# Kernel tuning notes

Measured on AMD Instinct MI355X. Metric: run time of the kernel, lower is better.

## Reference

```python
import jax, jax.numpy as jnp
import numpy as np

K = 32          # init k
E = 0.003       # EMA rate e


def setup_inputs() -> dict:
    key = jax.random.key(0)
    k1, _ = jax.random.split(key)
    features = jax.random.normal(k1, (512, 6, 8192), dtype=jnp.float32)
    threshold = jnp.zeros((1,), dtype=jnp.float32)
    return {"features": features, "threshold": threshold}


def reference(features, threshold):
    batch_size, n_layers, d_features = features.shape
    batch_k = K * batch_size * n_layers
    flat = features.reshape(-1)                      # [B*L*D]
    topk_vals, topk_idxs = jax.lax.top_k(flat, batch_k)
    topk_vals = jax.nn.relu(topk_vals)
    out = jnp.zeros_like(flat).at[topk_idxs].set(topk_vals)
    out = out.reshape(batch_size, n_layers, d_features)
    min_k = jax.lax.stop_gradient(jnp.min(topk_vals))
    new_threshold = (1.0 - E) * threshold + E * min_k
    return out, new_threshold
```

## Files before the change

### kernel.cpp

```cpp
#include <hip/hip_runtime.h>
#include <stdint.h>

#define K_TOTAL   98304u
#define EMA_RATE  0.003f

#define SBINS      16384
#define SBIN_SHIFT 18
#define SAMPLE_VEC 131072
#define STARGET    8192u
#define P2_BINS    4096
#define P2_SHIFT   12
#define LCAP       1024
#define CAP2       65536u
#define EQCAP      256

__device__ __forceinline__ unsigned f2key(float x) {
    unsigned u = __float_as_uint(x);
    return (u & 0x80000000u) ? ~u : (u | 0x80000000u);
}
__device__ __forceinline__ float key2f(unsigned key) {
    unsigned u = (key & 0x80000000u) ? (key & 0x7FFFFFFFu) : ~key;
    return __uint_as_float(u);
}

__global__ __launch_bounds__(256) void sample_hist_kernel(
        const float4* __restrict__ in, unsigned* __restrict__ shist) {
    __shared__ unsigned h[SBINS];
    for (int i = threadIdx.x; i < SBINS; i += 256) h[i] = 0;
    __syncthreads();
    int stride = gridDim.x * 256;
    for (int i = blockIdx.x * 256 + threadIdx.x; i < SAMPLE_VEC; i += stride) {
        float4 v = in[i];
        atomicAdd(&h[f2key(v.x) >> SBIN_SHIFT], 1u);
        atomicAdd(&h[f2key(v.y) >> SBIN_SHIFT], 1u);
        atomicAdd(&h[f2key(v.z) >> SBIN_SHIFT], 1u);
        atomicAdd(&h[f2key(v.w) >> SBIN_SHIFT], 1u);
    }
    __syncthreads();
    for (int i = threadIdx.x; i < SBINS; i += 256) {
        unsigned c = h[i];
        if (c) atomicAdd(&shist[i], c);
    }
}

__global__ __launch_bounds__(256) void sample_scan_kernel(
        const unsigned* __restrict__ shist, unsigned* __restrict__ res) {
    __shared__ unsigned psum[256];
    const int GB = SBINS / 256;
    int t = threadIdx.x;
    int hi = SBINS - 1 - t * GB;
    unsigned s = 0;
    for (int j = 0; j < GB; ++j) s += shist[hi - j];
    psum[t] = s;
    __syncthreads();
    for (int off = 1; off < 256; off <<= 1) {
        unsigned o = (t >= off) ? psum[t - off] : 0u;
        __syncthreads();
        psum[t] += o;
        __syncthreads();
    }
    unsigned cum = psum[t] - s;
    for (int j = 0; j < GB; ++j) {
        unsigned c = shist[hi - j];
        if (cum < STARGET && cum + c >= STARGET) {
            unsigned bin = (unsigned)(hi - j);
            unsigned bb = (bin > 0) ? bin - 1 : 0;
            res[0] = bb << SBIN_SHIFT;
        }
        cum += c;
    }
}

__global__ __launch_bounds__(256) void main_pass_kernel(
        const float4* __restrict__ in, const unsigned* __restrict__ res,
        float* __restrict__ cval, unsigned* __restrict__ cidx,
        unsigned* __restrict__ gcnt, unsigned* __restrict__ ghist,
        unsigned cap, int nvec) {
    __shared__ unsigned h[P2_BINS];
    __shared__ float    lval[LCAP];
    __shared__ unsigned lidx[LCAP];
    __shared__ unsigned lcnt, lbase;
    for (int i = threadIdx.x; i < P2_BINS; i += 256) h[i] = 0;
    if (threadIdx.x == 0) lcnt = 0;
    __syncthreads();
    unsigned base = res[0];
    int stride = gridDim.x * 256;
    for (int i = blockIdx.x * 256 + threadIdx.x; i < nvec; i += stride) {
        float4 v = in[i];
        unsigned idx = 4u * (unsigned)i;
        #pragma unroll
        for (int c = 0; c < 4; ++c) {
            float x = (c == 0) ? v.x : (c == 1) ? v.y : (c == 2) ? v.z : v.w;
            unsigned key = f2key(x);
            if (key >= base) {
                unsigned g = (key - base) >> P2_SHIFT;
                if (g > P2_BINS - 1) g = P2_BINS - 1;
                atomicAdd(&h[g], 1u);
                unsigned p = atomicAdd(&lcnt, 1u);
                if (p < LCAP) { lval[p] = x; lidx[p] = idx + c; }
                else {
                    unsigned q = atomicAdd(gcnt, 1u);
                    if (q < cap) { cval[q] = x; cidx[q] = idx + c; }
                }
            }
        }
    }
    __syncthreads();
    unsigned n = min(lcnt, (unsigned)LCAP);
    if (threadIdx.x == 0) lbase = atomicAdd(gcnt, n);
    __syncthreads();
    for (unsigned j = threadIdx.x; j < n; j += 256) {
        unsigned p = lbase + j;
        if (p < cap) { cval[p] = lval[j]; cidx[p] = lidx[j]; }
    }
    for (int i = threadIdx.x; i < P2_BINS; i += 256) {
        unsigned c = h[i];
        if (c) atomicAdd(&ghist[i], c);
    }
}

__global__ __launch_bounds__(256) void find_g_kernel(
        const unsigned* __restrict__ ghist, unsigned* __restrict__ res2) {
    __shared__ unsigned psum[256];
    const int GB = P2_BINS / 256;
    int t = threadIdx.x;
    int hi = P2_BINS - 1 - t * GB;
    unsigned s = 0;
    for (int j = 0; j < GB; ++j) s += ghist[hi - j];
    psum[t] = s;
    __syncthreads();
    for (int off = 1; off < 256; off <<= 1) {
        unsigned o = (t >= off) ? psum[t - off] : 0u;
        __syncthreads();
        psum[t] += o;
        __syncthreads();
    }
    unsigned cum = psum[t] - s;
    for (int j = 0; j < GB; ++j) {
        unsigned c = ghist[hi - j];
        if (cum < K_TOTAL && cum + c >= K_TOTAL) {
            res2[0] = (unsigned)(hi - j);
            res2[1] = K_TOTAL - cum;
        }
        cum += c;
    }
}

__global__ __launch_bounds__(256) void scatter_kernel(
        const float* __restrict__ cval, const unsigned* __restrict__ cidx,
        const unsigned* __restrict__ gcnt, const unsigned* __restrict__ res,
        const unsigned* __restrict__ res2,
        float* __restrict__ cval2, unsigned* __restrict__ cidx2,
        unsigned* __restrict__ cnt2, unsigned cap,
        float* __restrict__ out) {
    unsigned nc = min(*gcnt, cap);
    unsigned base = res[0];
    unsigned gstar = res2[0];
    int stride = gridDim.x * 256;
    for (unsigned i = blockIdx.x * 256 + threadIdx.x; i < nc; i += stride) {
        float x = cval[i];
        unsigned key = f2key(x);
        unsigned g = (key - base) >> P2_SHIFT;
        if (g > P2_BINS - 1) g = P2_BINS - 1;
        if (g > gstar) {
            out[cidx[i]] = fmaxf(x, 0.0f);
        } else if (g == gstar) {
            unsigned p = atomicAdd(cnt2, 1u);
            if (p < CAP2) { cval2[p] = x; cidx2[p] = cidx[i]; }
        }
    }
}

__global__ __launch_bounds__(256) void final_kernel(
        const float* __restrict__ cval2, const unsigned* __restrict__ cidx2,
        const unsigned* __restrict__ cnt2,
        const unsigned* __restrict__ res, const unsigned* __restrict__ res2,
        float* __restrict__ out,
        const float* __restrict__ thr_in, float* __restrict__ thr_out) {
    __shared__ unsigned h[1 << P2_SHIFT];
    __shared__ unsigned psum[256];
    __shared__ unsigned eqidx[EQCAP];
    __shared__ unsigned eqcnt;
    __shared__ unsigned sh_low, sh_need3;
    const int NB = 1 << P2_SHIFT;
    int t = threadIdx.x;
    unsigned nc2   = min(*cnt2, CAP2);
    unsigned base3 = res[0] + (res2[0] << P2_SHIFT);
    unsigned need2 = res2[1];

    for (int i = t; i < NB; i += 256) h[i] = 0;
    if (t == 0) eqcnt = 0;
    __syncthreads();
    for (unsigned i = t; i < nc2; i += 256) {
        unsigned low = f2key(cval2[i]) - base3;
        if (low > (unsigned)(NB - 1)) low = NB - 1;
        atomicAdd(&h[low], 1u);
    }
    __syncthreads();

    const int GB = NB / 256;
    int hi = NB - 1 - t * GB;
    unsigned s = 0;
    for (int j = 0; j < GB; ++j) s += h[hi - j];
    psum[t] = s;
    __syncthreads();
    for (int off = 1; off < 256; off <<= 1) {
        unsigned o = (t >= off) ? psum[t - off] : 0u;
        __syncthreads();
        psum[t] += o;
        __syncthreads();
    }
    unsigned cum = psum[t] - s;
    for (int j = 0; j < GB; ++j) {
        unsigned c = h[hi - j];
        if (cum < need2 && cum + c >= need2) {
            sh_low = (unsigned)(hi - j);
            sh_need3 = need2 - cum;
        }
        cum += c;
    }
    __syncthreads();
    unsigned kth_key = base3 + sh_low;
    unsigned need3   = sh_need3;

    for (unsigned i = t; i < nc2; i += 256) {
        float x = cval2[i];
        unsigned key = f2key(x);
        if (key > kth_key) {
            out[cidx2[i]] = fmaxf(x, 0.0f);
        } else if (key == kth_key) {
            unsigned p = atomicAdd(&eqcnt, 1u);
            if (p < EQCAP) eqidx[p] = cidx2[i];
        }
    }
    __syncthreads();

    unsigned ne = min(eqcnt, (unsigned)EQCAP);
    float vv = key2f(kth_key);
    for (unsigned e = t; e < ne; e += 256) {
        unsigned my = eqidx[e];
        unsigned rank = 0;
        for (unsigned f = 0; f < ne; ++f) rank += (eqidx[f] < my) ? 1u : 0u;
        if (rank < need3) out[my] = fmaxf(vv, 0.0f);
    }

    if (t == 0) {
        float mink = fmaxf(vv, 0.0f);
        thr_out[0] = (1.0f - EMA_RATE) * thr_in[0] + EMA_RATE * mink;
    }
}

extern "C" void kernel_launch(void* const* d_in, const int* in_sizes, int n_in,
                              void* d_out, int out_size, void* d_ws, size_t ws_size,
                              hipStream_t stream) {
    const float* feat   = (const float*)d_in[0];
    const float* thr_in = (const float*)d_in[1];
    float* out = (float*)d_out;
    int N    = in_sizes[0];
    int nvec = N / 4;

    uint8_t* w = (uint8_t*)d_ws;
    unsigned* shist = (unsigned*)w;
    unsigned* ghist = (unsigned*)(w + (64 << 10));
    unsigned* ctr   = (unsigned*)(w + (80 << 10));
    unsigned* gcnt  = ctr + 0;
    unsigned* cnt2  = ctr + 1;
    unsigned* res   = ctr + 4;
    unsigned* res2  = ctr + 8;

    size_t cand_off = (size_t)1 << 20;
    size_t avail    = (ws_size > cand_off + (CAP2 * 8 + 4096))
                        ? (ws_size - cand_off - CAP2 * 8 - 4096) / 8 : 0;
    unsigned cap = (unsigned)((avail < (size_t)(4u << 20)) ? avail : (size_t)(4u << 20));
    float*    cval  = (float*)(w + cand_off);
    unsigned* cidx  = (unsigned*)(w + cand_off + (size_t)cap * 4);
    float*    cval2 = (float*)(w + cand_off + (size_t)cap * 8);
    unsigned* cidx2 = (unsigned*)(w + cand_off + (size_t)cap * 8 + CAP2 * 4);

    hipMemsetAsync(d_ws, 0, (80 << 10) + 64, stream);
    hipMemsetAsync(d_out, 0, (size_t)N * 4, stream);

    sample_hist_kernel<<<128, 256, 0, stream>>>((const float4*)feat, shist);
    sample_scan_kernel<<<1,   256, 0, stream>>>(shist, res);
    main_pass_kernel  <<<1536, 256, 0, stream>>>((const float4*)feat, res,
                                                 cval, cidx, gcnt, ghist, cap, nvec);
    find_g_kernel     <<<1,   256, 0, stream>>>(ghist, res2);
    scatter_kernel    <<<64,  256, 0, stream>>>(cval, cidx, gcnt, res, res2,
                                                cval2, cidx2, cnt2, cap, out);
    final_kernel      <<<1,   256, 0, stream>>>(cval2, cidx2, cnt2, res, res2,
                                                out, thr_in, out + N);
}
```

Before: 266.3 us.

## Split candidate histogram out of main pass and unroll loads for memory parallelism

Moves the fine histogram off the full-input main pass into a separate kernel that runs only over the compacted candidates. This shrinks main-pass shared memory (no 4096-bin histogram) so more blocks can be resident. The main, sample and scatter loops are unrolled so several float4 loads are in flight per thread, and the single-block scan kernels widen to 1024 threads. The cost is one extra kernel launch and a second read of the candidate array.

```diff
diff --git a/kernel.cpp b/kernel.cpp
--- a/kernel.cpp
+++ b/kernel.cpp
@@ -14,6 +14,9 @@
 #define CAP2       65536u
 #define EQCAP      256
 
+#define MP_BLOCKS  3072
+#define MP_UNROLL  8
+
 __device__ __forceinline__ unsigned f2key(float x) {
     unsigned u = __float_as_uint(x);
     return (u & 0x80000000u) ? ~u : (u | 0x80000000u);
@@ -28,13 +31,23 @@
     __shared__ unsigned h[SBINS];
     for (int i = threadIdx.x; i < SBINS; i += 256) h[i] = 0;
     __syncthreads();
-    int stride = gridDim.x * 256;
-    for (int i = blockIdx.x * 256 + threadIdx.x; i < SAMPLE_VEC; i += stride) {
-        float4 v = in[i];
-        atomicAdd(&h[f2key(v.x) >> SBIN_SHIFT], 1u);
-        atomicAdd(&h[f2key(v.y) >> SBIN_SHIFT], 1u);
-        atomicAdd(&h[f2key(v.z) >> SBIN_SHIFT], 1u);
-        atomicAdd(&h[f2key(v.w) >> SBIN_SHIFT], 1u);
+    unsigned tid = blockIdx.x * 256 + threadIdx.x;
+    unsigned nth = gridDim.x * 256;
+    float4 v[4];
+    #pragma unroll
+    for (int u = 0; u < 4; ++u) {
+        unsigned j = tid + u * nth;
+        v[u] = (j < SAMPLE_VEC) ? in[j] : make_float4(0.f, 0.f, 0.f, 0.f);
+    }
+    #pragma unroll
+    for (int u = 0; u < 4; ++u) {
+        unsigned j = tid + u * nth;
+        if (j < SAMPLE_VEC) {
+            atomicAdd(&h[f2key(v[u].x) >> SBIN_SHIFT], 1u);
+            atomicAdd(&h[f2key(v[u].y) >> SBIN_SHIFT], 1u);
+            atomicAdd(&h[f2key(v[u].z) >> SBIN_SHIFT], 1u);
+            atomicAdd(&h[f2key(v[u].w) >> SBIN_SHIFT], 1u);
+        }
     }
     __syncthreads();
     for (int i = threadIdx.x; i < SBINS; i += 256) {
@@ -43,17 +56,22 @@
     }
 }
 
-__global__ __launch_bounds__(256) void sample_scan_kernel(
+__global__ __launch_bounds__(1024) void sample_scan_kernel(
         const unsigned* __restrict__ shist, unsigned* __restrict__ res) {
-    __shared__ unsigned psum[256];
-    const int GB = SBINS / 256;
+    __shared__ unsigned psum[1024];
+    const int T = 1024;
+    const int GB = SBINS / T;
     int t = threadIdx.x;
     int hi = SBINS - 1 - t * GB;
+    unsigned c[GB];
+    #pragma unroll
+    for (int j = 0; j < GB; ++j) c[j] = shist[hi - j];
     unsigned s = 0;
-    for (int j = 0; j < GB; ++j) s += shist[hi - j];
+    #pragma unroll
+    for (int j = 0; j < GB; ++j) s += c[j];
     psum[t] = s;
     __syncthreads();
-    for (int off = 1; off < 256; off <<= 1) {
+    for (int off = 1; off < T; off <<= 1) {
         unsigned o = (t >= off) ? psum[t - off] : 0u;
         __syncthreads();
         psum[t] += o;
@@ -61,46 +79,50 @@
     }
     unsigned cum = psum[t] - s;
     for (int j = 0; j < GB; ++j) {
-        unsigned c = shist[hi - j];
-        if (cum < STARGET && cum + c >= STARGET) {
+        if (cum < STARGET && cum + c[j] >= STARGET) {
             unsigned bin = (unsigned)(hi - j);
             unsigned bb = (bin > 0) ? bin - 1 : 0;
             res[0] = bb << SBIN_SHIFT;
         }
-        cum += c;
+        cum += c[j];
     }
 }
 
 __global__ __launch_bounds__(256) void main_pass_kernel(
         const float4* __restrict__ in, const unsigned* __restrict__ res,
         float* __restrict__ cval, unsigned* __restrict__ cidx,
-        unsigned* __restrict__ gcnt, unsigned* __restrict__ ghist,
-        unsigned cap, int nvec) {
-    __shared__ unsigned h[P2_BINS];
+        unsigned* __restrict__ gcnt, unsigned cap, int nvec) {
     __shared__ float    lval[LCAP];
     __shared__ unsigned lidx[LCAP];
     __shared__ unsigned lcnt, lbase;
-    for (int i = threadIdx.x; i < P2_BINS; i += 256) h[i] = 0;
     if (threadIdx.x == 0) lcnt = 0;
     __syncthreads();
     unsigned base = res[0];
-    int stride = gridDim.x * 256;
-    for (int i = blockIdx.x * 256 + threadIdx.x; i < nvec; i += stride) {
-        float4 v = in[i];
-        unsigned idx = 4u * (unsigned)i;
-        #pragma unroll
-        for (int c = 0; c < 4; ++c) {
-            float x = (c == 0) ? v.x : (c == 1) ? v.y : (c == 2) ? v.z : v.w;
-            unsigned key = f2key(x);
-            if (key >= base) {
-                unsigned g = (key - base) >> P2_SHIFT;
-                if (g > P2_BINS - 1) g = P2_BINS - 1;
-                atomicAdd(&h[g], 1u);
-                unsigned p = atomicAdd(&lcnt, 1u);
-                if (p < LCAP) { lval[p] = x; lidx[p] = idx + c; }
-                else {
-                    unsigned q = atomicAdd(gcnt, 1u);
-                    if (q < cap) { cval[q] = x; cidx[q] = idx + c; }
+    unsigned tid = blockIdx.x * 256 + threadIdx.x;
+    unsigned nth = gridDim.x * 256;
+    for (unsigned i0 = tid; i0 < (unsigned)nvec; i0 += MP_UNROLL * nth) {
+        float4 v[MP_UNROLL];
+        #pragma unroll
+        for (int u = 0; u < MP_UNROLL; ++u) {
+            unsigned j = i0 + u * nth;
+            v[u] = (j < (unsigned)nvec) ? in[j]
+                   : make_float4(-1e30f, -1e30f, -1e30f, -1e30f);
+        }
+        #pragma unroll
+        for (int u = 0; u < MP_UNROLL; ++u) {
+            unsigned j = i0 + u * nth;
+            unsigned idx = 4u * j;
+            float xs[4] = {v[u].x, v[u].y, v[u].z, v[u].w};
+            #pragma unroll
+            for (int c = 0; c < 4; ++c) {
+                unsigned key = f2key(xs[c]);
+                if (key >= base) {
+                    unsigned p = atomicAdd(&lcnt, 1u);
+                    if (p < LCAP) { lval[p] = xs[c]; lidx[p] = idx + c; }
+                    else {
+                        unsigned q = atomicAdd(gcnt, 1u);
+                        if (q < cap) { cval[q] = xs[c]; cidx[q] = idx + c; }
+                    }
                 }
             }
         }
@@ -113,23 +135,59 @@
         unsigned p = lbase + j;
         if (p < cap) { cval[p] = lval[j]; cidx[p] = lidx[j]; }
     }
+}
+
+__global__ __launch_bounds__(256) void cand_hist_kernel(
+        const float* __restrict__ cval, const unsigned* __restrict__ gcnt,
+        const unsigned* __restrict__ res, unsigned* __restrict__ ghist,
+        unsigned cap) {
+    __shared__ unsigned h[P2_BINS];
+    for (int i = threadIdx.x; i < P2_BINS; i += 256) h[i] = 0;
+    __syncthreads();
+    unsigned nc = min(*gcnt, cap);
+    unsigned base = res[0];
+    unsigned tid = blockIdx.x * 256 + threadIdx.x;
+    unsigned nth = gridDim.x * 256;
+    for (unsigned i0 = tid; i0 < nc; i0 += 4 * nth) {
+        float v[4];
+        #pragma unroll
+        for (int u = 0; u < 4; ++u) {
+            unsigned j = i0 + u * nth;
+            v[u] = (j < nc) ? cval[j] : -1e30f;
+        }
+        #pragma unroll
+        for (int u = 0; u < 4; ++u) {
+            unsigned j = i0 + u * nth;
+            if (j < nc) {
+                unsigned g = (f2key(v[u]) - base) >> P2_SHIFT;
+                if (g > P2_BINS - 1) g = P2_BINS - 1;
+                atomicAdd(&h[g], 1u);
+            }
+        }
+    }
+    __syncthreads();
     for (int i = threadIdx.x; i < P2_BINS; i += 256) {
         unsigned c = h[i];
         if (c) atomicAdd(&ghist[i], c);
     }
 }
 
-__global__ __launch_bounds__(256) void find_g_kernel(
+__global__ __launch_bounds__(1024) void find_g_kernel(
         const unsigned* __restrict__ ghist, unsigned* __restrict__ res2) {
-    __shared__ unsigned psum[256];
-    const int GB = P2_BINS / 256;
+    __shared__ unsigned psum[1024];
+    const int T = 1024;
+    const int GB = P2_BINS / T;
     int t = threadIdx.x;
     int hi = P2_BINS - 1 - t * GB;
+    unsigned c[GB];
+    #pragma unroll
+    for (int j = 0; j < GB; ++j) c[j] = ghist[hi - j];
     unsigned s = 0;
-    for (int j = 0; j < GB; ++j) s += ghist[hi - j];
+    #pragma unroll
+    for (int j = 0; j < GB; ++j) s += c[j];
     psum[t] = s;
     __syncthreads();
-    for (int off = 1; off < 256; off <<= 1) {
+    for (int off = 1; off < T; off <<= 1) {
         unsigned o = (t >= off) ? psum[t - off] : 0u;
         __syncthreads();
         psum[t] += o;
@@ -137,12 +195,11 @@
     }
     unsigned cum = psum[t] - s;
     for (int j = 0; j < GB; ++j) {
-        unsigned c = ghist[hi - j];
-        if (cum < K_TOTAL && cum + c >= K_TOTAL) {
+        if (cum < K_TOTAL && cum + c[j] >= K_TOTAL) {
             res2[0] = (unsigned)(hi - j);
             res2[1] = K_TOTAL - cum;
         }
-        cum += c;
+        cum += c[j];
     }
 }
 
@@ -156,17 +213,28 @@
     unsigned nc = min(*gcnt, cap);
     unsigned base = res[0];
     unsigned gstar = res2[0];
-    int stride = gridDim.x * 256;
-    for (unsigned i = blockIdx.x * 256 + threadIdx.x; i < nc; i += stride) {
-        float x = cval[i];
-        unsigned key = f2key(x);
-        unsigned g = (key - base) >> P2_SHIFT;
-        if (g > P2_BINS - 1) g = P2_BINS - 1;
-        if (g > gstar) {
-            out[cidx[i]] = fmaxf(x, 0.0f);
-        } else if (g == gstar) {
-            unsigned p = atomicAdd(cnt2, 1u);
-            if (p < CAP2) { cval2[p] = x; cidx2[p] = cidx[i]; }
+    unsigned tid = blockIdx.x * 256 + threadIdx.x;
+    unsigned nth = gridDim.x * 256;
+    for (unsigned i0 = tid; i0 < nc; i0 += 4 * nth) {
+        float v[4];
+        #pragma unroll
+        for (int u = 0; u < 4; ++u) {
+            unsigned j = i0 + u * nth;
+            v[u] = (j < nc) ? cval[j] : -1e30f;
+        }
+        #pragma unroll
+        for (int u = 0; u < 4; ++u) {
+            unsigned j = i0 + u * nth;
+            if (j < nc) {
+                unsigned g = (f2key(v[u]) - base) >> P2_SHIFT;
+                if (g > P2_BINS - 1) g = P2_BINS - 1;
+                if (g > gstar) {
+                    out[cidx[j]] = fmaxf(v[u], 0.0f);
+                } else if (g == gstar) {
+                    unsigned p = atomicAdd(cnt2, 1u);
+                    if (p < CAP2) { cval2[p] = v[u]; cidx2[p] = cidx[j]; }
+                }
+            }
         }
     }
 }
@@ -281,11 +349,12 @@
     hipMemsetAsync(d_out, 0, (size_t)N * 4, stream);
 
     sample_hist_kernel<<<128, 256, 0, stream>>>((const float4*)feat, shist);
-    sample_scan_kernel<<<1,   256, 0, stream>>>(shist, res);
-    main_pass_kernel  <<<1536, 256, 0, stream>>>((const float4*)feat, res,
-                                                 cval, cidx, gcnt, ghist, cap, nvec);
-    find_g_kernel     <<<1,   256, 0, stream>>>(ghist, res2);
-    scatter_kernel    <<<64,  256, 0, stream>>>(cval, cidx, gcnt, res, res2,
+    sample_scan_kernel<<<1,  1024, 0, stream>>>(shist, res);
+    main_pass_kernel  <<<MP_BLOCKS, 256, 0, stream>>>((const float4*)feat, res,
+                                                      cval, cidx, gcnt, cap, nvec);
+    cand_hist_kernel  <<<128, 256, 0, stream>>>(cval, gcnt, res, ghist, cap);
+    find_g_kernel     <<<1,  1024, 0, stream>>>(ghist, res2);
+    scatter_kernel    <<<128, 256, 0, stream>>>(cval, cidx, gcnt, res, res2,
                                                 cval2, cidx2, cnt2, cap, out);
     final_kernel      <<<1,   256, 0, stream>>>(cval2, cidx2, cnt2, res, res2,
                                                 out, thr_in, out + N);
```

New measurement: 238.4 us. 10.5% less time.
